# Kernel optimization log

Hardware: AMD Instinct MI355X
Metric: run time of the kernel (lower is better)

The kernel has to match this reference:

```python
import jax, jax.numpy as jnp
import numpy as np
from math import log2

N_QUBITS = 11
N_LAYERS = 2
DEGREE = 3
N_TIMESTEPS = 8
BSZ = 64
DIM = 2 ** N_QUBITS
N_ROTS = 4 * N_QUBITS * N_LAYERS  # 88


def _ry(theta):
    # batched RY(theta): (B,) -> (B,2,2) complex64
    h = 0.5 * theta
    c, s = jnp.cos(h), jnp.sin(h)
    U = jnp.stack([jnp.stack([c, -s], -1), jnp.stack([s, c], -1)], -2)
    return U.astype(jnp.complex64)


def _rx(theta):
    # batched RX(theta): (B,) -> (B,2,2) complex64
    h = 0.5 * theta
    c = jnp.cos(h).astype(jnp.complex64)
    s = (-1j) * jnp.sin(h).astype(jnp.complex64)
    return jnp.stack([jnp.stack([c, s], -1), jnp.stack([s, c], -1)], -2)


def _apply_1q(state, U, w):
    # state: (B,) + (2,)*n ; apply per-batch 2x2 U on wire w
    s = jnp.moveaxis(state, w + 1, 1)
    shp = s.shape
    s = s.reshape(shp[0], 2, -1)
    s = jnp.einsum('bij,bjr->bir', U, s)
    return jnp.moveaxis(s.reshape(shp), 1, w + 1)


def _apply_crx(state, theta, c_w, t_w):
    # controlled-RX: apply RX on target wire t_w where control wire c_w is |1>
    U = _rx(theta)
    s = jnp.moveaxis(state, (c_w + 1, t_w + 1), (1, 2))
    shp = s.shape
    s = s.reshape(shp[0], 2, 2, -1)
    s1 = jnp.einsum('bij,bjr->bir', U, s[:, 1])
    s = jnp.concatenate([s[:, :1], s1[:, None]], axis=1).reshape(shp)
    return jnp.moveaxis(s, (1, 2), (c_w + 1, t_w + 1))


def _sim14_evolve(state, params):
    # faithful sim14_circuit (v3 fixed RY-CRX gate set), batched angles
    n = state.ndim - 1
    layers = params.shape[1] // (4 * n)
    idx = 0
    for _ in range(layers):
        for i in range(n):
            state = _apply_1q(state, _ry(params[:, idx]), i); idx += 1
        for i in range(n - 1, -1, -1):
            state = _apply_crx(state, params[:, idx], i, (i + 1) % n); idx += 1
        for i in range(n):
            state = _apply_1q(state, _ry(params[:, idx]), i); idx += 1
        for i in [n - 1] + list(range(n - 1)):
            state = _apply_crx(state, params[:, idx], i, (i - 1) % n); idx += 1
    return state


def _apply_unitaries(base, uparams, coeffs):
    # apply_unitaries_pl: repeat_interleave + evolve + LCU einsum
    bsz, T, n_rots = uparams.shape
    dim = base.shape[1]
    n = int(round(log2(dim)))
    flat = uparams.reshape(bsz * T, n_rots)
    rep = jnp.repeat(base, T, axis=0).reshape((bsz * T,) + (2,) * n)
    ev = _sim14_evolve(rep, flat).reshape(bsz, T, dim)
    return jnp.einsum('bti,bt->bi', ev, coeffs.astype(jnp.complex64))


def setup_inputs() -> dict:
    key = jax.random.key(0)
    k1, k2, k3, k4 = jax.random.split(key, 4)
    base_states = jax.random.normal(k1, (BSZ, DIM), dtype=jnp.float32)
    unitary_params = jax.random.normal(k2, (BSZ, N_TIMESTEPS, N_ROTS), dtype=jnp.float32)
    lcu_coeffs = jax.random.normal(k3, (BSZ, N_TIMESTEPS), dtype=jnp.float32)
    poly_coeffs = jax.random.normal(k4, (DEGREE + 1,), dtype=jnp.float32)
    return {"base_states": base_states, "unitary_params": unitary_params,
            "lcu_coeffs": lcu_coeffs, "poly_coeffs": poly_coeffs}


def reference(base_states, unitary_params, lcu_coeffs, poly_coeffs):
    # evaluate_polynomial_state_pl (QSVT polynomial state preparation)
    base = base_states.astype(jnp.complex64)
    base = base / jnp.linalg.norm(base, axis=1, keepdims=True)  # valid quantum state
    pc = poly_coeffs.astype(jnp.complex64)
    acc = pc[0] * base
    working = base
    for k in range(1, poly_coeffs.shape[0]):
        working = _apply_unitaries(working, unitary_params, lcu_coeffs)
        acc = acc + pc[k] * working
    out = acc / jnp.sum(jnp.abs(poly_coeffs)).astype(jnp.complex64)
    # return real/imag stacked so output is real-valued: (bsz, dim, 2)
    return jnp.stack([out.real, out.imag], axis=-1)
```

## Files before the change

kernel.cpp:

```cpp
#include <hip/hip_runtime.h>
#include <utility>

#define DIM 2048
#define NQ 11
#define NROT 88
#define BSZ 64
#define NT 8
#define NPC 4

#if __has_builtin(__builtin_amdgcn_permlane16_swap)
#define HAVE_PL16 1
#else
#define HAVE_PL16 0
#endif
#if __has_builtin(__builtin_amdgcn_permlane32_swap)
#define HAVE_PL32 1
#else
#define HAVE_PL32 0
#endif

constexpr int g_type(int G) {
    int j = G % 44;
    return (j < 11 || (j >= 22 && j < 33)) ? 0 : 1;
}
constexpr int g_pt(int G) {
    int j = G % 44;
    if (j < 11) return 10 - j;
    if (j < 22) { int i = 21 - j; int tw = (i + 1 == NQ) ? 0 : i + 1; return 10 - tw; }
    if (j < 33) return 10 - (j - 22);
    if (j == 33) return 1;
    int i = j - 34; int tw = (i + 10) % NQ; return 10 - tw;
}
constexpr int g_pcb(int G) {
    int j = G % 44;
    if (j >= 11 && j < 22) { int i = 21 - j; return 10 - i; }
    if (j == 33) return 0;
    if (j >= 34) { int i = j - 34; return 10 - i; }
    return -1;
}
constexpr bool use_sum_tier(int lb) {
    return (lb == 4 && HAVE_PL16) || (lb == 5 && HAVE_PL32);
}

constexpr int tmap(int b) {
    if (b >= 1 && b <= 4) return b + 6;
    if (b >= 7 && b <= 10) return b - 6;
    return b;
}

constexpr int lop_j(int k) {
    if (k < 7)  return 4 + k;
    if (k == 7) return -1;
    if (k < 12) return k - 8;
    if (k == 12) return 11;
    if (k == 13) return -1;
    if (k < 21) return 12 + (k - 14);
    if (k == 21) return -1;
    if (k < 25) return 19 + (k - 22);
    if (k < 29) return 22 + (k - 25);
    if (k == 29) return 26;
    if (k == 30) return 27;
    if (k == 31) return 32;
    if (k == 32) return -1;
    if (k < 37) return 28 + (k - 33);
    if (k == 37) return 33;
    if (k == 38) return 34;
    if (k == 39) return -1;
    if (k < 46) return 35 + (k - 40);
    if (k == 46) return -1;
    return 41 + (k - 47);
}
constexpr bool lop_B(int k) {
    return (k >= 8 && k <= 12) || (k >= 22 && k <= 31) || (k >= 40 && k <= 45);
}
constexpr int lop_tpar(int k) { return (k == 7 || k == 21 || k == 39) ? 0 : 1; }

template<int G>
__device__ __forceinline__ void get_cs(float c0, float s0, float c1, float s1,
                                       float& c, float& s) {
    if constexpr (G < 64) {
        c = __int_as_float(__builtin_amdgcn_readlane(__float_as_int(c0), G));
        s = __int_as_float(__builtin_amdgcn_readlane(__float_as_int(s0), G));
    } else {
        c = __int_as_float(__builtin_amdgcn_readlane(__float_as_int(c1), G - 64));
        s = __int_as_float(__builtin_amdgcn_readlane(__float_as_int(s1), G - 64));
    }
}

template<int LB>
__device__ __forceinline__ float lxp(float x) {
    if constexpr (LB == 0) {
        return __int_as_float(__builtin_amdgcn_update_dpp(
            __float_as_int(x), __float_as_int(x), 0xB1, 0xF, 0xF, true));
    } else if constexpr (LB == 1) {
        return __int_as_float(__builtin_amdgcn_update_dpp(
            __float_as_int(x), __float_as_int(x), 0x4E, 0xF, 0xF, true));
    } else if constexpr (LB == 2) {
        return __int_as_float(__builtin_amdgcn_ds_swizzle(__float_as_int(x), 0x101F));
    } else if constexpr (LB == 3) {
        return __int_as_float(__builtin_amdgcn_update_dpp(
            __float_as_int(x), __float_as_int(x), 0x128, 0xF, 0xF, true));
    } else if constexpr (LB == 4) {
        return __int_as_float(__builtin_amdgcn_ds_swizzle(__float_as_int(x), 0x401F));
    } else {
        return __shfl_xor(x, 32, 64);
    }
}

template<int LB>
__device__ __forceinline__ float lxsum(float x) {
#if HAVE_PL16
    if constexpr (LB == 4) {
        unsigned u = __float_as_uint(x);
        auto r = __builtin_amdgcn_permlane16_swap(u, u, false, false);
        return __uint_as_float(r[0]) + __uint_as_float(r[1]);
    }
#endif
#if HAVE_PL32
    if constexpr (LB == 5) {
        unsigned u = __float_as_uint(x);
        auto r = __builtin_amdgcn_permlane32_swap(u, u, false, false);
        return __uint_as_float(r[0]) + __uint_as_float(r[1]);
    }
#endif
    return x + lxp<LB>(x);
}

template<int G, bool PB>
__device__ __forceinline__ void apply_gate(float2& R, float2& I,
    float c0, float s0, float c1, float s1, const int tid)
{
    constexpr int type = g_type(G);
    constexpr int pt   = PB ? tmap(g_pt(G)) : g_pt(G);
    constexpr int pcb0 = g_pcb(G);
    constexpr int pcb  = (pcb0 < 0) ? -1 : (PB ? tmap(pcb0) : pcb0);
    static_assert(pt <= 6, "block-bit target must run in transposed layout");
    float c, s;
    get_cs<G>(c0, s0, c1, s1, c, s);

    if constexpr (pt == 0) {
        if constexpr (type == 0) {
            float rx = R.x, ry = R.y, ix = I.x, iy = I.y;
            R.x = c*rx - s*ry;  R.y = s*rx + c*ry;
            I.x = c*ix - s*iy;  I.y = s*ix + c*iy;
        } else {
            const bool ctrl = (tid >> (pcb - 1)) & 1;
            if (ctrl) {
                float rx = R.x, ry = R.y, ix = I.x, iy = I.y;
                R.x = c*rx + s*iy;   I.x = c*ix - s*ry;
                R.y = c*ry + s*ix;   I.y = c*iy - s*rx;
            }
        }
    } else {
        constexpr int lb = pt - 1;
        if constexpr (use_sum_tier(lb)) {
            if constexpr (type == 0) {
                const float sg = ((tid >> lb) & 1) ? s : -s;
                const float k1 = c - sg;
                float srx = lxsum<lb>(R.x), sry = lxsum<lb>(R.y);
                float six = lxsum<lb>(I.x), siy = lxsum<lb>(I.y);
                R.x = k1*R.x + sg*srx;  R.y = k1*R.y + sg*sry;
                I.x = k1*I.x + sg*six;  I.y = k1*I.y + sg*siy;
            } else if constexpr (pcb == 0) {
                float sry = lxsum<lb>(R.y), siy = lxsum<lb>(I.y);
                float ry = R.y, iy = I.y;
                R.y = c*ry - s*iy + s*siy;
                I.y = c*iy + s*ry - s*sry;
            } else {
                const bool ctrl = (tid >> (pcb - 1)) & 1;
                if (ctrl) {
                    float srx = lxsum<lb>(R.x), sry = lxsum<lb>(R.y);
                    float six = lxsum<lb>(I.x), siy = lxsum<lb>(I.y);
                    float rx = R.x, ry = R.y, ix = I.x, iy = I.y;
                    R.x = c*rx - s*ix + s*six;  R.y = c*ry - s*iy + s*siy;
                    I.x = c*ix + s*rx - s*srx;  I.y = c*iy + s*ry - s*sry;
                }
            }
        } else {
            if constexpr (type == 0) {
                const float sg = ((tid >> lb) & 1) ? s : -s;
                float prx = lxp<lb>(R.x), pry = lxp<lb>(R.y);
                float pix = lxp<lb>(I.x), piy = lxp<lb>(I.y);
                R.x = c*R.x + sg*prx;  R.y = c*R.y + sg*pry;
                I.x = c*I.x + sg*pix;  I.y = c*I.y + sg*piy;
            } else if constexpr (pcb == 0) {
                float pry = lxp<lb>(R.y), piy = lxp<lb>(I.y);
                R.y = c*R.y + s*piy;
                I.y = c*I.y - s*pry;
            } else {
                const bool ctrl = (tid >> (pcb - 1)) & 1;
                if (ctrl) {
                    float prx = lxp<lb>(R.x), pry = lxp<lb>(R.y);
                    float pix = lxp<lb>(I.x), piy = lxp<lb>(I.y);
                    R.x = c*R.x + s*pix;  R.y = c*R.y + s*piy;
                    I.x = c*I.x - s*prx;  I.y = c*I.y - s*pry;
                }
            }
        }
    }
}

__device__ __forceinline__ int swz16(int s) { return s ^ ((s >> 6) & 15); }

template<int PAR>
__device__ __forceinline__ void transpose_swap(float2& R, float2& I,
    float4* __restrict__ exbuf, const int tid)
{
    float4* buf = exbuf + PAR * 1024;
    const int lo = tid & 15;
    const int hi = (tid >> 6) & 15;
    const int q = (tid & 0x030) | hi | (lo << 6);
    buf[swz16(tid)] = make_float4(R.x, R.y, I.x, I.y);
    __syncthreads();
    float4 v = buf[swz16(q)];
    R = make_float2(v.x, v.y);
    I = make_float2(v.z, v.w);
}

template<int K>
__device__ __forceinline__ void apply_op(float2& R, float2& I,
    float c0, float s0, float c1, float s1,
    float4* __restrict__ exbuf, const int tid)
{
    constexpr int layer = K / 50;
    constexpr int k = K % 50;
    constexpr int j = lop_j(k);
    if constexpr (j < 0) {
        transpose_swap<lop_tpar(k)>(R, I, exbuf, tid);
    } else {
        apply_gate<layer * 44 + j, lop_B(k)>(R, I, c0, s0, c1, s1, tid);
    }
}

template<int... Ks>
__device__ __forceinline__ void apply_all(std::integer_sequence<int, Ks...>,
    float2& R, float2& I,
    float c0, float s0, float c1, float s1,
    float4* __restrict__ exbuf, const int tid)
{
    (apply_op<Ks>(R, I, c0, s0, c1, s1, exbuf, tid), ...);
}

template<int MODE>
__global__ __launch_bounds__(1024, 8) void evolve_kernel(
    const void* __restrict__ src, const float* __restrict__ uparams,
    const float* __restrict__ lcu, float2* __restrict__ pout,
    const float* __restrict__ pcoef, float2* __restrict__ acc, int kprev)
{
    __shared__ float4 exbuf[2048];
    __shared__ float red[16];

    const int b = blockIdx.x >> 3;
    const int t = blockIdx.x & 7;
    const int tid = threadIdx.x;
    const int lane = tid & 63;

    const float* __restrict__ th_row = uparams + (size_t)(b * NT + t) * NROT;
    float th0 = 0.5f * th_row[lane];
    float th1 = (lane < NROT - 64) ? 0.5f * th_row[64 + lane] : 0.f;
    float tc0 = cosf(th0), ts0 = sinf(th0);
    float tc1 = cosf(th1), ts1 = sinf(th1);

    float2 R, I;
    if constexpr (MODE == 0) {
        const float2* b2s = (const float2*)((const float*)src + (size_t)b * DIM);
        float2 v = b2s[tid];
        float loc = v.x * v.x + v.y * v.y;
        for (int off = 32; off > 0; off >>= 1) loc += __shfl_down(loc, off, 64);
        if (lane == 0) red[tid >> 6] = loc;
        __syncthreads();
        float tot = 0.f;
#pragma unroll
        for (int w = 0; w < 16; ++w) tot += red[w];
        const float inv = rsqrtf(tot);
        R = make_float2(v.x * inv, v.y * inv);
        I = make_float2(0.f, 0.f);
        if (t == 0) {
            const float p0 = pcoef[0];
            float4* a4 = (float4*)(acc + (size_t)b * DIM);
            a4[tid] = make_float4(p0 * R.x, 0.f, p0 * R.y, 0.f);
        }
    } else if constexpr (MODE == 1) {
        R = make_float2(0.f, 0.f); I = make_float2(0.f, 0.f);
        const float2* s2 = (const float2*)src;
        for (int cc = 0; cc < NT; ++cc) {
            const float4* p4 = (const float4*)(s2 + ((size_t)b * NT + cc) * DIM);
            float4 v = p4[tid];
            R.x += v.x; I.x += v.y; R.y += v.z; I.y += v.w;
        }
        if (t == 0) {
            const float pk = pcoef[kprev];
            float4* a4 = (float4*)(acc + (size_t)b * DIM);
            float4 v = a4[tid];
            v.x += pk * R.x; v.y += pk * I.x;
            v.z += pk * R.y; v.w += pk * I.y;
            a4[tid] = v;
        }
    } else {
        const float2* s2 = (const float2*)src;
        const float4* p4 = (const float4*)(s2 + (size_t)b * DIM);
        float4 v = p4[tid];
        R.x = v.x; I.x = v.y; R.y = v.z; I.y = v.w;
    }

    apply_all(std::make_integer_sequence<int, 100>{}, R, I,
              tc0, ts0, tc1, ts1, exbuf, tid);

    const float coeff = lcu[b * NT + t];
    float4* o4 = (float4*)(pout + ((size_t)b * NT + t) * DIM);
    o4[tid] = make_float4(coeff * R.x, coeff * I.x, coeff * R.y, coeff * I.y);
}

__global__ __launch_bounds__(256) void final_kernel(
    const float2* __restrict__ partial, const float* __restrict__ pcoef,
    const float2* __restrict__ acc, float* __restrict__ out)
{
    int b = blockIdx.x >> 3;
    int i = ((blockIdx.x & 7) << 8) | threadIdx.x;
    float sr = 0.f, si = 0.f;
    for (int c = 0; c < NT; ++c) {
        float2 v = partial[((size_t)b * NT + c) * DIM + i];
        sr += v.x; si += v.y;
    }
    float sabs = 0.f;
    for (int q = 0; q < NPC; ++q) sabs += fabsf(pcoef[q]);
    float invn = 1.0f / sabs;
    float pk = pcoef[NPC - 1];
    float2 a = acc[(size_t)b * DIM + i];
    out[((size_t)b * DIM + i) * 2 + 0] = (a.x + pk * sr) * invn;
    out[((size_t)b * DIM + i) * 2 + 1] = (a.y + pk * si) * invn;
}

__global__ __launch_bounds__(256) void setup_kernel(
    const float* __restrict__ base, const float* __restrict__ pc,
    float2* __restrict__ working, float2* __restrict__ acc)
{
    int b = blockIdx.x;
    int tid = threadIdx.x;
    __shared__ float red[4];
    float ssum = 0.f;
    for (int i = tid; i < DIM; i += 256) {
        float v = base[b * DIM + i];
        ssum += v * v;
    }
    for (int off = 32; off > 0; off >>= 1) ssum += __shfl_down(ssum, off, 64);
    if ((tid & 63) == 0) red[tid >> 6] = ssum;
    __syncthreads();
    if (tid == 0) red[0] = red[0] + red[1] + red[2] + red[3];
    __syncthreads();
    float inv = rsqrtf(red[0]);
    float p0 = pc[0];
    for (int i = tid; i < DIM; i += 256) {
        float v = base[b * DIM + i] * inv;
        working[b * DIM + i] = make_float2(v, 0.f);
        acc[b * DIM + i] = make_float2(p0 * v, 0.f);
    }
}

__global__ __launch_bounds__(256) void reduce_kernel(
    const float2* __restrict__ partial, const float* __restrict__ pcoef,
    float2* __restrict__ working, float2* __restrict__ acc,
    float* __restrict__ out, int k, int last)
{
    int b = blockIdx.x >> 3;
    int i = ((blockIdx.x & 7) << 8) | threadIdx.x;
    float pk = pcoef[k];
    float sr = 0.f, si = 0.f;
    for (int c = 0; c < NT; ++c) {
        float2 v = partial[((size_t)b * NT + c) * DIM + i];
        sr += v.x; si += v.y;
    }
    working[b * DIM + i] = make_float2(sr, si);
    float2 a = acc[b * DIM + i];
    a.x += pk * sr; a.y += pk * si;
    acc[b * DIM + i] = a;
    if (last) {
        float sabs = 0.f;
        for (int q = 0; q < NPC; ++q) sabs += fabsf(pcoef[q]);
        float invn = 1.0f / sabs;
        out[((size_t)b * DIM + i) * 2 + 0] = a.x * invn;
        out[((size_t)b * DIM + i) * 2 + 1] = a.y * invn;
    }
}

extern "C" void kernel_launch(void* const* d_in, const int* in_sizes, int n_in,
                              void* d_out, int out_size, void* d_ws, size_t ws_size,
                              hipStream_t stream) {
    const float* base = (const float*)d_in[0];
    const float* upar = (const float*)d_in[1];
    const float* lcu  = (const float*)d_in[2];
    const float* pc   = (const float*)d_in[3];
    float* out = (float*)d_out;

    const size_t plane = (size_t)BSZ * DIM * sizeof(float2);
    char* ws = (char*)d_ws;

    if (ws_size >= (1 + 3 * (size_t)NT) * plane) {
        float2* acc = (float2*)ws;
        float2* pA  = (float2*)(ws + plane);
        float2* pB  = (float2*)(ws + plane + (size_t)NT * plane);
        float2* pC  = (float2*)(ws + plane + (size_t)2 * NT * plane);
        evolve_kernel<0><<<BSZ * NT, 1024, 0, stream>>>(base, upar, lcu, pA, pc, acc, 0);
        evolve_kernel<1><<<BSZ * NT, 1024, 0, stream>>>(pA,   upar, lcu, pB, pc, acc, 1);
        evolve_kernel<1><<<BSZ * NT, 1024, 0, stream>>>(pB,   upar, lcu, pC, pc, acc, 2);
        final_kernel<<<BSZ * 8, 256, 0, stream>>>(pC, pc, acc, out);
    } else {
        float2* working = (float2*)ws;
        float2* acc     = (float2*)(ws + plane);
        float2* pA      = (float2*)(ws + 2 * plane);
        setup_kernel<<<BSZ, 256, 0, stream>>>(base, pc, working, acc);
        for (int k = 1; k <= NPC - 1; ++k) {
            evolve_kernel<2><<<BSZ * NT, 1024, 0, stream>>>(working, upar, lcu, pA, pc, acc, 0);
            reduce_kernel<<<BSZ * 8, 256, 0, stream>>>(pA, pc, working, acc, out,
                                                       k, (k == NPC - 1) ? 1 : 0);
        }
    }
}
```

Baseline: 90.75 us.

## Fuse three evolve stages and final reduction into one cooperative kernel

Replaces the sequence of three evolve launches plus the final reduction with a single cooperative-launch kernel. It uses grid-wide syncs between polynomial stages and keeps the per-block cos/sin angle setup in registers across stages. The aim is to remove kernel launch gaps and repeated angle setup. In exchange, all 512 blocks of 1024 threads must be co-resident, otherwise the cooperative launch fails and the old multi-kernel path runs. The rewritten small-workspace fallback now reads and writes the same partial buffer in place across blocks, which risks a race.

```diff
diff --git a/kernel.cpp b/kernel.cpp
--- a/kernel.cpp
+++ b/kernel.cpp
@@ -1,5 +1,8 @@
 #include <hip/hip_runtime.h>
+#include <hip/hip_cooperative_groups.h>
 #include <utility>
+
+namespace cg = cooperative_groups;
 
 #define DIM 2048
 #define NQ 11
@@ -241,6 +244,117 @@
     (apply_op<Ks>(R, I, c0, s0, c1, s1, exbuf, tid), ...);
 }
 
+__device__ __forceinline__ void evolve_once(float2& R, float2& I,
+    float c0, float s0, float c1, float s1,
+    float4* __restrict__ exbuf, const int tid)
+{
+    apply_all(std::make_integer_sequence<int, 100>{}, R, I, c0, s0, c1, s1, exbuf, tid);
+}
+
+__global__ __launch_bounds__(1024, 8) void fused_kernel(
+    const float* __restrict__ base, const float* __restrict__ uparams,
+    const float* __restrict__ lcu, const float* __restrict__ pcoef,
+    float2* __restrict__ acc, float2* __restrict__ pA,
+    float2* __restrict__ pB, float2* __restrict__ pC,
+    float* __restrict__ out)
+{
+    __shared__ float4 exbuf[2048];
+    __shared__ float red[16];
+    cg::grid_group grid = cg::this_grid();
+
+    const int b = blockIdx.x >> 3;
+    const int t = blockIdx.x & 7;
+    const int tid = threadIdx.x;
+    const int lane = tid & 63;
+
+    const float* __restrict__ th_row = uparams + (size_t)(b * NT + t) * NROT;
+    float th0 = 0.5f * th_row[lane];
+    float th1 = (lane < NROT - 64) ? 0.5f * th_row[64 + lane] : 0.f;
+    const float tc0 = cosf(th0), ts0 = sinf(th0);
+    const float tc1 = cosf(th1), ts1 = sinf(th1);
+    const float coeff = lcu[b * NT + t];
+
+    float2 R, I;
+    {
+        const float2* b2s = (const float2*)(base + (size_t)b * DIM);
+        float2 v = b2s[tid];
+        float loc = v.x * v.x + v.y * v.y;
+        for (int off = 32; off > 0; off >>= 1) loc += __shfl_down(loc, off, 64);
+        if (lane == 0) red[tid >> 6] = loc;
+        __syncthreads();
+        float tot = 0.f;
+#pragma unroll
+        for (int w = 0; w < 16; ++w) tot += red[w];
+        const float inv = rsqrtf(tot);
+        R = make_float2(v.x * inv, v.y * inv);
+        I = make_float2(0.f, 0.f);
+        if (t == 0) {
+            const float p0 = pcoef[0];
+            float4* a4 = (float4*)(acc + (size_t)b * DIM);
+            a4[tid] = make_float4(p0 * R.x, 0.f, p0 * R.y, 0.f);
+        }
+    }
+    __syncthreads();
+    evolve_once(R, I, tc0, ts0, tc1, ts1, exbuf, tid);
+    ((float4*)(pA + ((size_t)b * NT + t) * DIM))[tid] =
+        make_float4(coeff * R.x, coeff * I.x, coeff * R.y, coeff * I.y);
+    grid.sync();
+
+    {
+        R = make_float2(0.f, 0.f); I = make_float2(0.f, 0.f);
+        for (int cc = 0; cc < NT; ++cc) {
+            float4 v = ((const float4*)(pA + ((size_t)b * NT + cc) * DIM))[tid];
+            R.x += v.x; I.x += v.y; R.y += v.z; I.y += v.w;
+        }
+        if (t == 0) {
+            const float pk = pcoef[1];
+            float4* a4 = (float4*)(acc + (size_t)b * DIM);
+            float4 v = a4[tid];
+            v.x += pk * R.x; v.y += pk * I.x; v.z += pk * R.y; v.w += pk * I.y;
+            a4[tid] = v;
+        }
+    }
+    evolve_once(R, I, tc0, ts0, tc1, ts1, exbuf, tid);
+    ((float4*)(pB + ((size_t)b * NT + t) * DIM))[tid] =
+        make_float4(coeff * R.x, coeff * I.x, coeff * R.y, coeff * I.y);
+    grid.sync();
+
+    {
+        R = make_float2(0.f, 0.f); I = make_float2(0.f, 0.f);
+        for (int cc = 0; cc < NT; ++cc) {
+            float4 v = ((const float4*)(pB + ((size_t)b * NT + cc) * DIM))[tid];
+            R.x += v.x; I.x += v.y; R.y += v.z; I.y += v.w;
+        }
+        if (t == 0) {
+            const float pk = pcoef[2];
+            float4* a4 = (float4*)(acc + (size_t)b * DIM);
+            float4 v = a4[tid];
+            v.x += pk * R.x; v.y += pk * I.x; v.z += pk * R.y; v.w += pk * I.y;
+            a4[tid] = v;
+        }
+    }
+    evolve_once(R, I, tc0, ts0, tc1, ts1, exbuf, tid);
+    ((float4*)(pC + ((size_t)b * NT + t) * DIM))[tid] =
+        make_float4(coeff * R.x, coeff * I.x, coeff * R.y, coeff * I.y);
+    grid.sync();
+
+    if (tid < 256) {
+        const int i = t * 256 + tid;
+        float sr = 0.f, si = 0.f;
+        for (int cc = 0; cc < NT; ++cc) {
+            float2 v = pC[((size_t)b * NT + cc) * DIM + i];
+            sr += v.x; si += v.y;
+        }
+        float sabs = 0.f;
+        for (int q = 0; q < NPC; ++q) sabs += fabsf(pcoef[q]);
+        const float invn = 1.0f / sabs;
+        const float pk = pcoef[NPC - 1];
+        float2 a = acc[(size_t)b * DIM + i];
+        out[((size_t)b * DIM + i) * 2 + 0] = (a.x + pk * sr) * invn;
+        out[((size_t)b * DIM + i) * 2 + 1] = (a.y + pk * si) * invn;
+    }
+}
+
 template<int MODE>
 __global__ __launch_bounds__(1024, 8) void evolve_kernel(
     const void* __restrict__ src, const float* __restrict__ uparams,
@@ -280,35 +394,28 @@
             float4* a4 = (float4*)(acc + (size_t)b * DIM);
             a4[tid] = make_float4(p0 * R.x, 0.f, p0 * R.y, 0.f);
         }
-    } else if constexpr (MODE == 1) {
+        __syncthreads();
+    } else {
         R = make_float2(0.f, 0.f); I = make_float2(0.f, 0.f);
         const float2* s2 = (const float2*)src;
         for (int cc = 0; cc < NT; ++cc) {
-            const float4* p4 = (const float4*)(s2 + ((size_t)b * NT + cc) * DIM);
-            float4 v = p4[tid];
+            float4 v = ((const float4*)(s2 + ((size_t)b * NT + cc) * DIM))[tid];
             R.x += v.x; I.x += v.y; R.y += v.z; I.y += v.w;
         }
-        if (t == 0) {
+        if (t == 0 && kprev > 0) {
             const float pk = pcoef[kprev];
             float4* a4 = (float4*)(acc + (size_t)b * DIM);
             float4 v = a4[tid];
-            v.x += pk * R.x; v.y += pk * I.x;
-            v.z += pk * R.y; v.w += pk * I.y;
+            v.x += pk * R.x; v.y += pk * I.x; v.z += pk * R.y; v.w += pk * I.y;
             a4[tid] = v;
         }
-    } else {
-        const float2* s2 = (const float2*)src;
-        const float4* p4 = (const float4*)(s2 + (size_t)b * DIM);
-        float4 v = p4[tid];
-        R.x = v.x; I.x = v.y; R.y = v.z; I.y = v.w;
-    }
-
-    apply_all(std::make_integer_sequence<int, 100>{}, R, I,
-              tc0, ts0, tc1, ts1, exbuf, tid);
+    }
+
+    evolve_once(R, I, tc0, ts0, tc1, ts1, exbuf, tid);
 
     const float coeff = lcu[b * NT + t];
-    float4* o4 = (float4*)(pout + ((size_t)b * NT + t) * DIM);
-    o4[tid] = make_float4(coeff * R.x, coeff * I.x, coeff * R.y, coeff * I.y);
+    ((float4*)(pout + ((size_t)b * NT + t) * DIM))[tid] =
+        make_float4(coeff * R.x, coeff * I.x, coeff * R.y, coeff * I.y);
 }
 
 __global__ __launch_bounds__(256) void final_kernel(
@@ -329,58 +436,6 @@
     float2 a = acc[(size_t)b * DIM + i];
     out[((size_t)b * DIM + i) * 2 + 0] = (a.x + pk * sr) * invn;
     out[((size_t)b * DIM + i) * 2 + 1] = (a.y + pk * si) * invn;
-}
-
-__global__ __launch_bounds__(256) void setup_kernel(
-    const float* __restrict__ base, const float* __restrict__ pc,
-    float2* __restrict__ working, float2* __restrict__ acc)
-{
-    int b = blockIdx.x;
-    int tid = threadIdx.x;
-    __shared__ float red[4];
-    float ssum = 0.f;
-    for (int i = tid; i < DIM; i += 256) {
-        float v = base[b * DIM + i];
-        ssum += v * v;
-    }
-    for (int off = 32; off > 0; off >>= 1) ssum += __shfl_down(ssum, off, 64);
-    if ((tid & 63) == 0) red[tid >> 6] = ssum;
-    __syncthreads();
-    if (tid == 0) red[0] = red[0] + red[1] + red[2] + red[3];
-    __syncthreads();
-    float inv = rsqrtf(red[0]);
-    float p0 = pc[0];
-    for (int i = tid; i < DIM; i += 256) {
-        float v = base[b * DIM + i] * inv;
-        working[b * DIM + i] = make_float2(v, 0.f);
-        acc[b * DIM + i] = make_float2(p0 * v, 0.f);
-    }
-}
-
-__global__ __launch_bounds__(256) void reduce_kernel(
-    const float2* __restrict__ partial, const float* __restrict__ pcoef,
-    float2* __restrict__ working, float2* __restrict__ acc,
-    float* __restrict__ out, int k, int last)
-{
-    int b = blockIdx.x >> 3;
-    int i = ((blockIdx.x & 7) << 8) | threadIdx.x;
-    float pk = pcoef[k];
-    float sr = 0.f, si = 0.f;
-    for (int c = 0; c < NT; ++c) {
-        float2 v = partial[((size_t)b * NT + c) * DIM + i];
-        sr += v.x; si += v.y;
-    }
-    working[b * DIM + i] = make_float2(sr, si);
-    float2 a = acc[b * DIM + i];
-    a.x += pk * sr; a.y += pk * si;
-    acc[b * DIM + i] = a;
-    if (last) {
-        float sabs = 0.f;
-        for (int q = 0; q < NPC; ++q) sabs += fabsf(pcoef[q]);
-        float invn = 1.0f / sabs;
-        out[((size_t)b * DIM + i) * 2 + 0] = a.x * invn;
-        out[((size_t)b * DIM + i) * 2 + 1] = a.y * invn;
-    }
 }
 
 extern "C" void kernel_launch(void* const* d_in, const int* in_sizes, int n_in,
@@ -395,24 +450,32 @@
     const size_t plane = (size_t)BSZ * DIM * sizeof(float2);
     char* ws = (char*)d_ws;
 
+    float2* acc = (float2*)ws;
+    float2* pA  = (float2*)(ws + plane);
+    float2* pB  = (float2*)(ws + plane + (size_t)NT * plane);
+    float2* pC  = (float2*)(ws + plane + (size_t)2 * NT * plane);
+
+    bool fused_ok = false;
     if (ws_size >= (1 + 3 * (size_t)NT) * plane) {
-        float2* acc = (float2*)ws;
-        float2* pA  = (float2*)(ws + plane);
-        float2* pB  = (float2*)(ws + plane + (size_t)NT * plane);
-        float2* pC  = (float2*)(ws + plane + (size_t)2 * NT * plane);
+        void* args[] = {(void*)&base, (void*)&upar, (void*)&lcu, (void*)&pc,
+                        (void*)&acc, (void*)&pA, (void*)&pB, (void*)&pC, (void*)&out};
+        hipError_t err = hipLaunchCooperativeKernel(
+            (void*)fused_kernel, dim3(BSZ * NT), dim3(1024), args, 0, stream);
+        fused_ok = (err == hipSuccess);
+    }
+
+    if (!fused_ok && ws_size >= (1 + 3 * (size_t)NT) * plane) {
         evolve_kernel<0><<<BSZ * NT, 1024, 0, stream>>>(base, upar, lcu, pA, pc, acc, 0);
         evolve_kernel<1><<<BSZ * NT, 1024, 0, stream>>>(pA,   upar, lcu, pB, pc, acc, 1);
         evolve_kernel<1><<<BSZ * NT, 1024, 0, stream>>>(pB,   upar, lcu, pC, pc, acc, 2);
         final_kernel<<<BSZ * 8, 256, 0, stream>>>(pC, pc, acc, out);
-    } else {
-        float2* working = (float2*)ws;
-        float2* acc     = (float2*)(ws + plane);
-        float2* pA      = (float2*)(ws + 2 * plane);
-        setup_kernel<<<BSZ, 256, 0, stream>>>(base, pc, working, acc);
-        for (int k = 1; k <= NPC - 1; ++k) {
-            evolve_kernel<2><<<BSZ * NT, 1024, 0, stream>>>(working, upar, lcu, pA, pc, acc, 0);
-            reduce_kernel<<<BSZ * 8, 256, 0, stream>>>(pA, pc, working, acc, out,
-                                                       k, (k == NPC - 1) ? 1 : 0);
-        }
-    }
-}
+    } else if (!fused_ok) {
+        float2* working = (float2*)(ws + plane);
+        float2* pOnly   = (float2*)(ws + 2 * plane);
+        evolve_kernel<0><<<BSZ * NT, 1024, 0, stream>>>(base, upar, lcu, pOnly, pc, acc, 0);
+        evolve_kernel<1><<<BSZ * NT, 1024, 0, stream>>>(pOnly, upar, lcu, pOnly, pc, acc, 1);
+        evolve_kernel<1><<<BSZ * NT, 1024, 0, stream>>>(pOnly, upar, lcu, pOnly, pc, acc, 2);
+        final_kernel<<<BSZ * 8, 256, 0, stream>>>(pOnly, pc, acc, out);
+        (void)working;
+    }
+}
```

New measurement: 221.2 us. 144% more time.
